# Kernel tuning notes

Hardware: AMD Instinct MI355X
Metric: run time of the kernel (lower is better)

The kernel has to match this reference:

```python
import jax, jax.numpy as jnp
import numpy as np

B, T, C, H = 8, 2048, 1024, 128  # batch, seq (== block_size), embed dim, head size


def setup_inputs() -> dict:
    key = jax.random.key(0)
    kx, kq, kk, kv = jax.random.split(key, 4)
    x = jax.random.normal(kx, (B, T, C), dtype=jnp.float32)
    # torch Linear(no bias) weights: [head_size, in_features], applied as x @ W.T
    s = 1.0 / np.sqrt(C)
    Wq = jax.random.normal(kq, (H, C), dtype=jnp.float32) * s
    Wk = jax.random.normal(kk, (H, C), dtype=jnp.float32) * s
    Wv = jax.random.normal(kv, (H, C), dtype=jnp.float32) * s
    return {"x": x, "Wq": Wq, "Wk": Wk, "Wv": Wv}


def reference(x, Wq, Wk, Wv):
    # projections: [B,T,C] @ [C,H] -> [B,T,H]
    q = jnp.einsum('btc,hc->bth', x, Wq)
    k = jnp.einsum('btc,hc->bth', x, Wk)
    v = jnp.einsum('btc,hc->bth', x, Wv)
    scale = k.shape[-1] ** -0.5
    # scores [B,T,T], causal mask, softmax in fp32 (autocast disabled in original)
    scores = jnp.einsum('bqh,bkh->bqk', q, k) * scale
    causal = jnp.tril(jnp.ones((T, T), dtype=bool))
    scores = jnp.where(causal, scores, -jnp.inf)
    attn = jax.nn.softmax(scores.astype(jnp.float32), axis=-1)
    # dropout_rate = 0.0 -> identity
    out = jnp.einsum('bqk,bkh->bqh', attn.astype(v.dtype), v)
    return out
```

## Files before the change

kernel.cpp:

```cpp
#include <hip/hip_runtime.h>
#include <hip/hip_bf16.h>

constexpr int NB = 8;
constexpr int T  = 2048;
constexpr int C  = 1024;
constexpr int Hd = 128;

typedef short bf16x8 __attribute__((ext_vector_type(8)));
typedef float floatx4 __attribute__((ext_vector_type(4)));

__device__ __forceinline__ ushort f2bf(float x) {
    return __builtin_bit_cast(ushort, __float2bfloat16(x));
}
__device__ __forceinline__ float bf2f(ushort u) {
    unsigned int x = ((unsigned int)u) << 16;
    return __builtin_bit_cast(float, x);
}
__device__ __forceinline__ void async16(ushort* lds, const ushort* g) {
    __builtin_amdgcn_global_load_lds(
        (const __attribute__((address_space(1))) unsigned int*)g,
        (__attribute__((address_space(3))) unsigned int*)lds, 16, 0, 0);
}

__global__ __launch_bounds__(256) void convert_xw(
    const float* __restrict__ X, const float* __restrict__ Wq,
    const float* __restrict__ Wk, const float* __restrict__ Wv,
    ushort* __restrict__ Xb, ushort* __restrict__ Wb)
{
    int bid = blockIdx.x;
    if (bid < 8192) {
        size_t i = ((size_t)bid * 256 + threadIdx.x) * 8;
        float4 a = *(const float4*)&X[i];
        float4 b = *(const float4*)&X[i + 4];
        bf16x8 o;
        o[0] = (short)f2bf(a.x); o[1] = (short)f2bf(a.y);
        o[2] = (short)f2bf(a.z); o[3] = (short)f2bf(a.w);
        o[4] = (short)f2bf(b.x); o[5] = (short)f2bf(b.y);
        o[6] = (short)f2bf(b.z); o[7] = (short)f2bf(b.w);
        *(bf16x8*)&Xb[i] = o;
    } else {
        int g = (bid - 8192) * 256 + threadIdx.x;
        size_t base = (size_t)g * 8;
        int sel = (int)(base >> 17);
        const float* W = sel == 0 ? Wq : (sel == 1 ? Wk : Wv);
        float s = (sel == 0) ? 0.12751744f : 1.0f;
        size_t off = base - (size_t)sel * 131072;
        float4 a = *(const float4*)&W[off];
        float4 b = *(const float4*)&W[off + 4];
        bf16x8 o;
        o[0] = (short)f2bf(a.x * s); o[1] = (short)f2bf(a.y * s);
        o[2] = (short)f2bf(a.z * s); o[3] = (short)f2bf(a.w * s);
        o[4] = (short)f2bf(b.x * s); o[5] = (short)f2bf(b.y * s);
        o[6] = (short)f2bf(b.z * s); o[7] = (short)f2bf(b.w * s);
        *(bf16x8*)&Wb[base] = o;
    }
}

__global__ __launch_bounds__(256) void qkv_gemm(
    const ushort* __restrict__ Xb, const ushort* __restrict__ Wb,
    ushort* __restrict__ Qo, ushort* __restrict__ Ko, ushort* __restrict__ Vt)
{
    __shared__ ushort SM[24576];
    ushort* Al = SM;
    ushort* Bl = SM + 16384;
    const int m0 = blockIdx.x * 128;
    const int n0 = blockIdx.y * 64;
    const int tid = threadIdx.x, lane = tid & 63, wave = tid >> 6;
    const int quad = lane >> 4, colL = lane & 15;
    const int wm = (wave & 1) * 64, wn = (wave >> 1) * 32;
    const int lr4 = lane >> 4;
    const int cg  = lane & 15;

    floatx4 acc[4][2] = {};

    for (int k0 = 0; k0 < C; k0 += 128) {
        for (int t = 0; t < 8; ++t) {
            int q = wave * 8 + t;
            int row = q * 4 + lr4;
            async16(&Al[q * 512 + lane * 8],
                    &Xb[(size_t)(m0 + row) * C + k0 + ((cg ^ (row & 7)) * 8)]);
        }
        for (int t = 0; t < 4; ++t) {
            int q = wave * 4 + t;
            int row = q * 4 + lr4;
            async16(&Bl[q * 512 + lane * 8],
                    &Wb[(size_t)(n0 + row) * C + k0 + ((cg ^ (row & 7)) * 8)]);
        }
        __syncthreads();

        for (int kk = 0; kk < 4; ++kk) {
            bf16x8 af[4], bfr[2];
            for (int mt = 0; mt < 4; ++mt)
                af[mt] = *(const bf16x8*)
                    &Al[(wm + mt * 16 + colL) * 128 + (((kk * 4 + quad) ^ (colL & 7))) * 8];
            for (int nt = 0; nt < 2; ++nt)
                bfr[nt] = *(const bf16x8*)
                    &Bl[(wn + nt * 16 + colL) * 128 + (((kk * 4 + quad) ^ (colL & 7))) * 8];
            for (int mt = 0; mt < 4; ++mt)
                for (int nt = 0; nt < 2; ++nt)
                    acc[mt][nt] = __builtin_amdgcn_mfma_f32_16x16x32_bf16(
                        af[mt], bfr[nt], acc[mt][nt], 0, 0, 0);
        }
        __syncthreads();
    }

    const int sel = n0 >> 7;
    const int h0 = n0 & 127;
    if (sel < 2) {
        ushort* dst = sel == 0 ? Qo : Ko;
        for (int mt = 0; mt < 4; ++mt)
            for (int nt = 0; nt < 2; ++nt)
                for (int r = 0; r < 4; ++r) {
                    int row = m0 + wm + mt * 16 + quad * 4 + r;
                    int h = h0 + wn + nt * 16 + colL;
                    dst[(size_t)row * Hd + h] = f2bf(acc[mt][nt][r]);
                }
    } else {
        ushort* TL = SM;
        for (int mt = 0; mt < 4; ++mt)
            for (int nt = 0; nt < 2; ++nt)
                for (int r = 0; r < 4; ++r)
                    TL[(wm + mt * 16 + quad * 4 + r) * 66 + wn + nt * 16 + colL] =
                        f2bf(acc[mt][nt][r]);
        __syncthreads();
        const int b = m0 >> 11, tb = m0 & 2047;
        const int h = tid & 63, tq = tid >> 6;
        for (int st = 0; st < 4; ++st) {
            int t0 = tq * 32 + st * 8;
            bf16x8 o;
            for (int jx = 0; jx < 8; ++jx)
                o[jx] = (short)TL[(t0 + jx) * 66 + h];
            *(bf16x8*)&Vt[((size_t)b * Hd + h0 + h) * T + tb + t0] = o;
        }
    }
}

__global__ __launch_bounds__(256, 2) void attn_partial(
    const ushort* __restrict__ Q, const ushort* __restrict__ Kg,
    const ushort* __restrict__ Vt, ushort* __restrict__ Opart,
    float* __restrict__ lpart)
{
    __shared__ ushort Kl[128 * 128];
    __shared__ ushort Vl[128 * 128];

    const int tid = threadIdx.x, lane = tid & 63, wave = tid >> 6;
    const int quad = lane >> 4, colL = lane & 15;

    const int id = blockIdx.x;
    const int s  = id & 3;
    const int bq = id >> 2;
    const int b  = bq & 7;
    const int qt = 31 - (bq >> 3);
    const int q0 = qt * 64;
    const int cmax = (q0 + 63) >> 7;

    const int r16 = tid >> 4, p16 = tid & 15;

    bf16x8 qa[4];
    {
        const ushort* qp =
            &Q[((size_t)b * T + q0 + wave * 16 + colL) * Hd + quad * 8];
        for (int ks = 0; ks < 4; ++ks)
            qa[ks] = *(const bf16x8*)&qp[ks * 32];
    }

    floatx4 Oacc[8] = {};
    float l_p[4] = {0.f, 0.f, 0.f, 0.f};

    if (s <= cmax) {
        {
            const int k0 = s * 128;
            for (int t = 0; t < 8; ++t) {
                int row = t * 16 + r16;
                async16(&Kl[t * 2048 + tid * 8],
                        &Kg[((size_t)b * T + k0 + row) * Hd + ((p16 ^ (row & 15)) * 8)]);
            }
            for (int t = 0; t < 8; ++t) {
                int hrow = t * 16 + r16;
                async16(&Vl[t * 2048 + tid * 8],
                        &Vt[((size_t)b * Hd + hrow) * T + k0 + ((p16 ^ (hrow & 15)) * 8)]);
            }
        }

        for (int c = s; c <= cmax; c += 4) {
            __syncthreads();

            floatx4 accS[8] = {};
            for (int ks = 0; ks < 4; ++ks)
                for (int nt = 0; nt < 8; ++nt) {
                    int krow = nt * 16 + colL;
                    bf16x8 kb = *(const bf16x8*)
                        &Kl[krow * 128 + (((ks * 4 + quad) ^ colL) * 8)];
                    accS[nt] = __builtin_amdgcn_mfma_f32_16x16x32_bf16(qa[ks], kb, accS[nt], 0, 0, 0);
                }

            if (c == cmax) {
                const int k0 = c * 128;
                for (int nt = 0; nt < 8; ++nt)
                    for (int rr = 0; rr < 4; ++rr) {
                        int lrow = q0 + wave * 16 + quad * 4 + rr;
                        int lcol = k0 + nt * 16 + colL;
                        if (lcol > lrow) accS[nt][rr] = -__builtin_inff();
                    }
            }
            __syncthreads();

            ushort* Pw = &Kl[wave * 2048];
            for (int nt = 0; nt < 8; ++nt)
                for (int rr = 0; rr < 4; ++rr) {
                    float p = __builtin_amdgcn_exp2f(fminf(accS[nt][rr], 14.f));
                    l_p[rr] += p;
                    int prow = quad * 4 + rr;
                    Pw[prow * 128 + ((nt * 16 + colL) ^ ((prow & 7) << 4))] = f2bf(p);
                }

            bf16x8 pa[4];
            {
                const int prow = colL;
                const int sw = (prow & 7) << 4;
                for (int ks = 0; ks < 4; ++ks)
                    pa[ks] = *(const bf16x8*)&Pw[prow * 128 + ((ks * 32 + quad * 8) ^ sw)];
            }
            __syncthreads();

            if (c + 4 <= cmax) {
                const int k0 = (c + 4) * 128;
                for (int t = 0; t < 8; ++t) {
                    int row = t * 16 + r16;
                    async16(&Kl[t * 2048 + tid * 8],
                            &Kg[((size_t)b * T + k0 + row) * Hd + ((p16 ^ (row & 15)) * 8)]);
                }
            }

            for (int ks = 0; ks < 4; ++ks)
                for (int th = 0; th < 8; ++th) {
                    int hrow = th * 16 + colL;
                    bf16x8 vb = *(const bf16x8*)
                        &Vl[hrow * 128 + (((ks * 4 + quad) ^ colL) * 8)];
                    Oacc[th] = __builtin_amdgcn_mfma_f32_16x16x32_bf16(pa[ks], vb, Oacc[th], 0, 0, 0);
                }

            if (c + 4 <= cmax) {
                __syncthreads();
                const int k0 = (c + 4) * 128;
                for (int t = 0; t < 8; ++t) {
                    int hrow = t * 16 + r16;
                    async16(&Vl[t * 2048 + tid * 8],
                            &Vt[((size_t)b * Hd + hrow) * T + k0 + ((p16 ^ (hrow & 15)) * 8)]);
                }
            }
        }
    }

    float l_r[4];
    for (int rr = 0; rr < 4; ++rr) {
        float v = l_p[rr];
        for (int off = 1; off < 16; off <<= 1)
            v += __shfl_xor(v, off, 64);
        l_r[rr] = v;
    }
    ushort* Op = &Opart[(size_t)id * 8192];
    for (int th = 0; th < 8; ++th)
        for (int rr = 0; rr < 4; ++rr) {
            int row = wave * 16 + quad * 4 + rr;
            Op[row * 128 + th * 16 + colL] = f2bf(Oacc[th][rr]);
        }
    if (colL == 0)
        for (int rr = 0; rr < 4; ++rr) {
            int row = wave * 16 + quad * 4 + rr;
            lpart[(size_t)id * 64 + row] = l_r[rr];
        }
}

__global__ __launch_bounds__(256) void attn_combine(
    const ushort* __restrict__ Opart, const float* __restrict__ lpart,
    float* __restrict__ out)
{
    const int bq = blockIdx.x;
    const int b  = bq & 7;
    const int qt = 31 - (bq >> 3);
    const int t = threadIdx.x;
    const int row_l = t >> 2;
    const int c32 = (t & 3) * 32;

    float l = 0.f;
    for (int s = 0; s < 4; ++s)
        l += lpart[(size_t)(bq * 4 + s) * 64 + row_l];
    const float inv = 1.0f / l;

    float acc[32];
#pragma unroll
    for (int i = 0; i < 32; ++i) acc[i] = 0.f;
    for (int s = 0; s < 4; ++s) {
        const ushort* p = &Opart[(size_t)(bq * 4 + s) * 8192 + row_l * 128 + c32];
#pragma unroll
        for (int x = 0; x < 4; ++x) {
            bf16x8 a = *(const bf16x8*)&p[x * 8];
#pragma unroll
            for (int i2 = 0; i2 < 8; ++i2)
                acc[x * 8 + i2] += bf2f((ushort)a[i2]);
        }
    }
    float* dst = &out[((size_t)b * T + qt * 64 + row_l) * Hd + c32];
#pragma unroll
    for (int x = 0; x < 8; ++x) {
        float4 o;
        o.x = acc[x * 4 + 0] * inv;
        o.y = acc[x * 4 + 1] * inv;
        o.z = acc[x * 4 + 2] * inv;
        o.w = acc[x * 4 + 3] * inv;
        *(float4*)&dst[x * 4] = o;
    }
}

extern "C" void kernel_launch(void* const* d_in, const int* in_sizes, int n_in,
                              void* d_out, int out_size, void* d_ws, size_t ws_size,
                              hipStream_t stream) {
    const float* x  = (const float*)d_in[0];
    const float* Wq = (const float*)d_in[1];
    const float* Wk = (const float*)d_in[2];
    const float* Wv = (const float*)d_in[3];
    float* out = (float*)d_out;

    char* w = (char*)d_ws;
    ushort* Xb = (ushort*)w;
    ushort* Opart = (ushort*)w;
    float* lpart  = (float*)(w + (size_t)1024 * 8192 * 2);
    w += (size_t)33554432;
    ushort* Wb = (ushort*)w;  w += (size_t)786432;
    ushort* Qb  = (ushort*)w;  w += (size_t)NB * T * Hd * 2;
    ushort* Kb  = (ushort*)w;  w += (size_t)NB * T * Hd * 2;
    ushort* Vtb = (ushort*)w;  w += (size_t)NB * T * Hd * 2;

    convert_xw<<<8384, 256, 0, stream>>>(x, Wq, Wk, Wv, Xb, Wb);
    qkv_gemm<<<dim3(128, 6), 256, 0, stream>>>(Xb, Wb, Qb, Kb, Vtb);
    attn_partial<<<1024, 256, 0, stream>>>(Qb, Kb, Vtb, Opart, lpart);
    attn_combine<<<256, 256, 0, stream>>>(Opart, lpart, out);
}
```

Measured before the change: 149.1 us.

## Double-buffer QKV GEMM loads and widen N tile to full head

The QKV projection GEMM now uses 128x128 output tiles (one full Q, K or V head per block), so the grid drops from 768 to 384 blocks. K slices shrink to 64 and are double-buffered in LDS so the async global-to-LDS copy of the next slice overlaps the MFMA work on the current one. Each wave now does a 64x64 sub-tile, which raises register use and leaves fewer blocks to fill the GPU's compute units.

```diff
diff --git a/kernel.cpp b/kernel.cpp
--- a/kernel.cpp
+++ b/kernel.cpp
@@ -60,77 +60,86 @@
     const ushort* __restrict__ Xb, const ushort* __restrict__ Wb,
     ushort* __restrict__ Qo, ushort* __restrict__ Ko, ushort* __restrict__ Vt)
 {
-    __shared__ ushort SM[24576];
-    ushort* Al = SM;
-    ushort* Bl = SM + 16384;
+    __shared__ ushort SM[32768];
     const int m0 = blockIdx.x * 128;
-    const int n0 = blockIdx.y * 64;
+    const int n0 = blockIdx.y * 128;
     const int tid = threadIdx.x, lane = tid & 63, wave = tid >> 6;
     const int quad = lane >> 4, colL = lane & 15;
-    const int wm = (wave & 1) * 64, wn = (wave >> 1) * 32;
-    const int lr4 = lane >> 4;
-    const int cg  = lane & 15;
-
-    floatx4 acc[4][2] = {};
-
-    for (int k0 = 0; k0 < C; k0 += 128) {
-        for (int t = 0; t < 8; ++t) {
-            int q = wave * 8 + t;
-            int row = q * 4 + lr4;
-            async16(&Al[q * 512 + lane * 8],
-                    &Xb[(size_t)(m0 + row) * C + k0 + ((cg ^ (row & 7)) * 8)]);
-        }
-        for (int t = 0; t < 4; ++t) {
-            int q = wave * 4 + t;
-            int row = q * 4 + lr4;
-            async16(&Bl[q * 512 + lane * 8],
-                    &Wb[(size_t)(n0 + row) * C + k0 + ((cg ^ (row & 7)) * 8)]);
-        }
+    const int wm = (wave & 1) * 64, wn = (wave >> 1) * 64;
+    const int lr = lane >> 3;
+    const int lcs = ((lane & 7) ^ (lr & 7)) * 8;
+
+    floatx4 acc[4][4] = {};
+
+    #define QKV_STAGE(buf, kt)                                                   \
+        {                                                                        \
+            const int k0_ = (kt) * 64;                                           \
+            ushort* Ab_ = SM + (buf) * 16384;                                    \
+            ushort* Bb_ = SM + (buf) * 16384 + 8192;                             \
+            for (int t = 0; t < 4; ++t) {                                        \
+                int q = wave * 4 + t;                                            \
+                async16(&Ab_[q * 512 + lane * 8],                                \
+                        &Xb[(size_t)(m0 + q * 8 + lr) * C + k0_ + lcs]);         \
+            }                                                                    \
+            for (int t = 0; t < 4; ++t) {                                        \
+                int q = wave * 4 + t;                                            \
+                async16(&Bb_[q * 512 + lane * 8],                                \
+                        &Wb[(size_t)(n0 + q * 8 + lr) * C + k0_ + lcs]);         \
+            }                                                                    \
+        }
+
+    QKV_STAGE(0, 0)
+
+    for (int kt = 0; kt < 16; ++kt) {
+        const int cur = kt & 1;
         __syncthreads();
 
-        for (int kk = 0; kk < 4; ++kk) {
-            bf16x8 af[4], bfr[2];
+        if (kt + 1 < 16) QKV_STAGE(cur ^ 1, kt + 1)
+
+        const ushort* Ab = SM + cur * 16384;
+        const ushort* Bb = SM + cur * 16384 + 8192;
+        for (int kk = 0; kk < 2; ++kk) {
+            bf16x8 af[4], bfr[4];
+            const int g = ((kk * 4 + quad) ^ (colL & 7)) * 8;
             for (int mt = 0; mt < 4; ++mt)
-                af[mt] = *(const bf16x8*)
-                    &Al[(wm + mt * 16 + colL) * 128 + (((kk * 4 + quad) ^ (colL & 7))) * 8];
-            for (int nt = 0; nt < 2; ++nt)
-                bfr[nt] = *(const bf16x8*)
-                    &Bl[(wn + nt * 16 + colL) * 128 + (((kk * 4 + quad) ^ (colL & 7))) * 8];
+                af[mt] = *(const bf16x8*)&Ab[(wm + mt * 16 + colL) * 64 + g];
+            for (int nt = 0; nt < 4; ++nt)
+                bfr[nt] = *(const bf16x8*)&Bb[(wn + nt * 16 + colL) * 64 + g];
             for (int mt = 0; mt < 4; ++mt)
-                for (int nt = 0; nt < 2; ++nt)
+                for (int nt = 0; nt < 4; ++nt)
                     acc[mt][nt] = __builtin_amdgcn_mfma_f32_16x16x32_bf16(
                         af[mt], bfr[nt], acc[mt][nt], 0, 0, 0);
         }
-        __syncthreads();
-    }
+    }
+    #undef QKV_STAGE
 
     const int sel = n0 >> 7;
-    const int h0 = n0 & 127;
     if (sel < 2) {
         ushort* dst = sel == 0 ? Qo : Ko;
         for (int mt = 0; mt < 4; ++mt)
-            for (int nt = 0; nt < 2; ++nt)
+            for (int nt = 0; nt < 4; ++nt)
                 for (int r = 0; r < 4; ++r) {
                     int row = m0 + wm + mt * 16 + quad * 4 + r;
-                    int h = h0 + wn + nt * 16 + colL;
+                    int h = wn + nt * 16 + colL;
                     dst[(size_t)row * Hd + h] = f2bf(acc[mt][nt][r]);
                 }
     } else {
+        __syncthreads();
         ushort* TL = SM;
         for (int mt = 0; mt < 4; ++mt)
-            for (int nt = 0; nt < 2; ++nt)
+            for (int nt = 0; nt < 4; ++nt)
                 for (int r = 0; r < 4; ++r)
-                    TL[(wm + mt * 16 + quad * 4 + r) * 66 + wn + nt * 16 + colL] =
+                    TL[(wm + mt * 16 + quad * 4 + r) * 130 + wn + nt * 16 + colL] =
                         f2bf(acc[mt][nt][r]);
         __syncthreads();
         const int b = m0 >> 11, tb = m0 & 2047;
-        const int h = tid & 63, tq = tid >> 6;
-        for (int st = 0; st < 4; ++st) {
-            int t0 = tq * 32 + st * 8;
+        const int h = tid & 127, tq = tid >> 7;
+        for (int st = 0; st < 8; ++st) {
+            int t0 = tq * 64 + st * 8;
             bf16x8 o;
             for (int jx = 0; jx < 8; ++jx)
-                o[jx] = (short)TL[(t0 + jx) * 66 + h];
-            *(bf16x8*)&Vt[((size_t)b * Hd + h0 + h) * T + tb + t0] = o;
+                o[jx] = (short)TL[(t0 + jx) * 130 + h];
+            *(bf16x8*)&Vt[((size_t)b * Hd + h) * T + tb + t0] = o;
         }
     }
 }
@@ -333,7 +342,7 @@
     ushort* Vtb = (ushort*)w;  w += (size_t)NB * T * Hd * 2;
 
     convert_xw<<<8384, 256, 0, stream>>>(x, Wq, Wk, Wv, Xb, Wb);
-    qkv_gemm<<<dim3(128, 6), 256, 0, stream>>>(Xb, Wb, Qb, Kb, Vtb);
+    qkv_gemm<<<dim3(128, 3), 256, 0, stream>>>(Xb, Wb, Qb, Kb, Vtb);
     attn_partial<<<1024, 256, 0, stream>>>(Qb, Kb, Vtb, Opart, lpart);
     attn_combine<<<256, 256, 0, stream>>>(Opart, lpart, out);
 }
```

Result: no change. 150.9 us (+1.2%).
